# Optimization experiments

Measured on AMD Instinct MI355X. Metric: run time of the kernel, lower is better.

## Reference

```python
import jax, jax.numpy as jnp
import numpy as np

B, S, R, D_NODE, D_PAIR, N_HEAD, C = 1, 128, 256, 256, 128, 8, 32
EPS = 1e-5


def layer_norm(x, g, b):
    mu = jnp.mean(x, axis=-1, keepdims=True)
    var = jnp.mean(jnp.square(x - mu), axis=-1, keepdims=True)
    return (x - mu) * jax.lax.rsqrt(var + EPS) * g + b


def self_attention(x, qkv_w, qkv_b, gate_w, gate_b, o_w, o_b, bias=None):
    # x: [B, n1, n2, d]; attends over n2. heads: n_head x c, n_head*c == d.
    b_, n1, n2, d = x.shape
    qkv = x @ qkv_w.T + qkv_b                      # [B, n1, n2, 3*h*c]
    q, k, v = jnp.split(qkv, 3, axis=-1)
    split_heads = lambda t: t.reshape(b_, n1, n2, N_HEAD, C).transpose(0, 1, 3, 2, 4)  # [B,n1,h,n2,c]
    q = split_heads(q) * (C ** -0.5)
    k = split_heads(k)
    v = split_heads(v)
    logits = jnp.einsum('bshqc,bshkc->bshqk', q, k)  # [B, n1, h, n2, n2]
    if bias is not None:
        logits = logits + bias[:, None]              # bias: [B, h, n2, n2]
    w = jax.nn.softmax(logits, axis=-1)
    o = jnp.einsum('bshqk,bshkc->bshqc', w, v)
    o = o.transpose(0, 1, 3, 2, 4).reshape(b_, n1, n2, N_HEAD * C)
    gate = jax.nn.sigmoid(x @ gate_w.T + gate_b)
    o = o * gate
    out = o @ o_w.T
    if o_b is not None:
        out = out + o_b
    return out


def setup_inputs() -> dict:
    key = jax.random.key(0)
    ks = jax.random.split(key, 12)
    rn = lambda k, sh, sc=1.0: jax.random.normal(k, sh, dtype=jnp.float32) * sc
    return {
        'node': rn(ks[0], (B, S, R, D_NODE)),
        'pair': rn(ks[1], (B, R, R, D_PAIR)),
        'ln_mr_g': jnp.ones((D_NODE,), jnp.float32), 'ln_mr_b': jnp.zeros((D_NODE,), jnp.float32),
        'ln_z_g': jnp.ones((D_PAIR,), jnp.float32), 'ln_z_b': jnp.zeros((D_PAIR,), jnp.float32),
        'b_weights': rn(ks[2], (N_HEAD, D_PAIR), D_PAIR ** -0.5),
        'row_qkv_w': rn(ks[3], (3 * N_HEAD * C, D_NODE), D_NODE ** -0.5),
        'row_qkv_b': jnp.zeros((3 * N_HEAD * C,), jnp.float32),
        'row_gate_w': rn(ks[4], (N_HEAD * C, D_NODE), D_NODE ** -0.5),
        'row_gate_b': jnp.ones((N_HEAD * C,), jnp.float32),
        'row_o_w': rn(ks[5], (D_NODE, N_HEAD * C), D_NODE ** -0.5),
        'out_bias': jnp.zeros((D_NODE,), jnp.float32),
        'ln_mc_g': jnp.ones((D_NODE,), jnp.float32), 'ln_mc_b': jnp.zeros((D_NODE,), jnp.float32),
        'col_qkv_w': rn(ks[6], (3 * N_HEAD * C, D_NODE), D_NODE ** -0.5),
        'col_qkv_b': jnp.zeros((3 * N_HEAD * C,), jnp.float32),
        'col_gate_w': rn(ks[7], (N_HEAD * C, D_NODE), D_NODE ** -0.5),
        'col_gate_b': jnp.ones((N_HEAD * C,), jnp.float32),
        'col_o_w': rn(ks[8], (D_NODE, N_HEAD * C), D_NODE ** -0.5),
        'col_o_b': jnp.zeros((D_NODE,), jnp.float32),
        'ln_t_g': jnp.ones((D_NODE,), jnp.float32), 'ln_t_b': jnp.zeros((D_NODE,), jnp.float32),
        't_w1': rn(ks[9], (4 * D_NODE, D_NODE), D_NODE ** -0.5),
        't_b1': jnp.zeros((4 * D_NODE,), jnp.float32),
        't_w2': rn(ks[10], (D_NODE, 4 * D_NODE), (4 * D_NODE) ** -0.5),
        't_b2': jnp.zeros((D_NODE,), jnp.float32),
    }


def reference(node, pair, ln_mr_g, ln_mr_b, ln_z_g, ln_z_b, b_weights,
              row_qkv_w, row_qkv_b, row_gate_w, row_gate_b, row_o_w, out_bias,
              ln_mc_g, ln_mc_b, col_qkv_w, col_qkv_b, col_gate_w, col_gate_b, col_o_w, col_o_b,
              ln_t_g, ln_t_b, t_w1, t_b1, t_w2, t_b2):
    # --- MSARowAttentionWithPairBias ---
    M = layer_norm(node, ln_mr_g, ln_mr_b)                 # [B,S,R,D]
    Z = layer_norm(pair, ln_z_g, ln_z_b)                   # [B,R,R,Dp]
    b = jnp.einsum('bqkd,hd->bhqk', Z, b_weights)          # pair bias [B,h,R,R]
    M = self_attention(M, row_qkv_w, row_qkv_b, row_gate_w, row_gate_b, row_o_w, None, bias=b)
    # bias_dropout_add with ones dropout mask (inference): residual + (x + bias)
    node = node + M + out_bias
    # --- MSAColumnAttention ---
    Mt = node.transpose(0, 2, 1, 3)                        # [B,R,S,D], attend over S
    Mt = layer_norm(Mt, ln_mc_g, ln_mc_b)
    Mt = self_attention(Mt, col_qkv_w, col_qkv_b, col_gate_w, col_gate_b, col_o_w, col_o_b)
    node = node + Mt.transpose(0, 2, 1, 3)
    # --- MSATransition (n=4) ---
    x = layer_norm(node, ln_t_g, ln_t_b)
    x = jax.nn.relu(x @ t_w1.T + t_b1) @ t_w2.T + t_b2
    return node + x
```

## Files before the change

### kernel.cpp

```cpp
#include <hip/hip_runtime.h>
#include <hip/hip_bf16.h>

#define EPS 1e-5f

typedef __hip_bfloat16 bf16;
typedef __attribute__((ext_vector_type(8))) short short8v;
typedef __attribute__((ext_vector_type(4))) short short4v;
typedef __attribute__((ext_vector_type(4))) float f32x4;

__device__ inline f32x4 mfma16bf(short4v a, short4v b, f32x4 c) {
#if __has_builtin(__builtin_amdgcn_mfma_f32_16x16x16bf16_1k)
  return __builtin_amdgcn_mfma_f32_16x16x16bf16_1k(a, b, c, 0, 0, 0);
#else
  short8v a8 = {a[0], a[1], a[2], a[3], 0, 0, 0, 0};
  short8v b8 = {b[0], b[1], b[2], b[3], 0, 0, 0, 0};
  return __builtin_amdgcn_mfma_f32_16x16x32_bf16(a8, b8, c, 0, 0, 0);
#endif
}

__device__ inline void load_lds16(const void* g, void* l) {
  __builtin_amdgcn_global_load_lds(
      (const __attribute__((address_space(1))) void*)g,
      (__attribute__((address_space(3))) void*)l, 16, 0, 0);
}

__device__ inline unsigned pack_bf16x2(float a, float b) {
  union { bf16 h[2]; unsigned u; } cv;
  cv.h[0] = __float2bfloat16(a);
  cv.h[1] = __float2bfloat16(b);
  return cv.u;
}

struct CvtArgs {
  const float* src[8];
  bf16* dst[8];
  int n4[8];
};

__global__ __launch_bounds__(256) void cvt_all_kernel(CvtArgs a) {
  int i = blockIdx.x * 256 + threadIdx.x;
#pragma unroll
  for (int s = 0; s < 8; ++s) {
    if (i < a.n4[s]) {
      float4 v = reinterpret_cast<const float4*>(a.src[s])[i];
      union { ushort4 u; bf16 h[4]; } cv;
      cv.h[0] = __float2bfloat16(v.x);
      cv.h[1] = __float2bfloat16(v.y);
      cv.h[2] = __float2bfloat16(v.z);
      cv.h[3] = __float2bfloat16(v.w);
      reinterpret_cast<ushort4*>(a.dst[s])[i] = cv.u;
      return;
    }
    i -= a.n4[s];
  }
}

__global__ __launch_bounds__(256) void bias_concat_kernel(
    const float* rq, const float* rg, const float* cq, const float* cg,
    float* br, float* bc) {
  int i = blockIdx.x * 256 + threadIdx.x;
  if (i < 1024) {
    br[i] = (i < 768) ? rq[i] : rg[i - 768];
  } else {
    int j = i - 1024;
    bc[j] = (j < 768) ? cq[j] : cg[j - 768];
  }
}

__global__ __launch_bounds__(512) void ln256_bf_kernel(
    const float* __restrict__ in, bf16* __restrict__ out,
    const float* __restrict__ g, const float* __restrict__ b) {
  int tid = threadIdx.x;
  int w = tid >> 6, lane = tid & 63;
  int row0 = blockIdx.x * 16 + w * 2;
  const float4* r0 = reinterpret_cast<const float4*>(in + (size_t)row0 * 256);
  const float4* r1 =
      reinterpret_cast<const float4*>(in + (size_t)(row0 + 1) * 256);
  float4 x0 = r0[lane];
  float4 x1 = r1[lane];
  float4 gv = reinterpret_cast<const float4*>(g)[lane];
  float4 bv = reinterpret_cast<const float4*>(b)[lane];

  float s0 = x0.x + x0.y + x0.z + x0.w;
  float q0 = x0.x * x0.x + x0.y * x0.y + x0.z * x0.z + x0.w * x0.w;
  float s1 = x1.x + x1.y + x1.z + x1.w;
  float q1 = x1.x * x1.x + x1.y * x1.y + x1.z * x1.z + x1.w * x1.w;
#pragma unroll
  for (int off = 32; off >= 1; off >>= 1) {
    s0 += __shfl_xor(s0, off);
    q0 += __shfl_xor(q0, off);
    s1 += __shfl_xor(s1, off);
    q1 += __shfl_xor(q1, off);
  }
  float m0 = s0 * (1.0f / 256.0f);
  float i0 = rsqrtf(q0 * (1.0f / 256.0f) - m0 * m0 + EPS);
  float m1 = s1 * (1.0f / 256.0f);
  float i1 = rsqrtf(q1 * (1.0f / 256.0f) - m1 * m1 + EPS);

  union { ushort4 u; bf16 h[4]; } c0, c1;
  c0.h[0] = __float2bfloat16((x0.x - m0) * i0 * gv.x + bv.x);
  c0.h[1] = __float2bfloat16((x0.y - m0) * i0 * gv.y + bv.y);
  c0.h[2] = __float2bfloat16((x0.z - m0) * i0 * gv.z + bv.z);
  c0.h[3] = __float2bfloat16((x0.w - m0) * i0 * gv.w + bv.w);
  c1.h[0] = __float2bfloat16((x1.x - m1) * i1 * gv.x + bv.x);
  c1.h[1] = __float2bfloat16((x1.y - m1) * i1 * gv.y + bv.y);
  c1.h[2] = __float2bfloat16((x1.z - m1) * i1 * gv.z + bv.z);
  c1.h[3] = __float2bfloat16((x1.w - m1) * i1 * gv.w + bv.w);
  reinterpret_cast<ushort4*>(out + (size_t)row0 * 256)[lane] = c0.u;
  reinterpret_cast<ushort4*>(out + (size_t)(row0 + 1) * 256)[lane] = c1.u;
}

__global__ __launch_bounds__(256) void pair_bias_kernel(
    const float* __restrict__ pair, const float* __restrict__ g,
    const float* __restrict__ b, const float* __restrict__ bw,
    bf16* __restrict__ bT) {
  int tid = threadIdx.x;
  int w = tid >> 6, lane = tid & 63;
  int l15 = lane & 15, l4 = lane >> 4;
  int rowbase = blockIdx.x * 64 + w * 16;
  const float* zrow = pair + (size_t)(rowbase + l15) * 128;

  float z[4][8];
#pragma unroll
  for (int kk = 0; kk < 4; ++kk) {
    float4 a0 = *reinterpret_cast<const float4*>(zrow + kk * 32 + l4 * 8);
    float4 a1 = *reinterpret_cast<const float4*>(zrow + kk * 32 + l4 * 8 + 4);
    z[kk][0] = a0.x; z[kk][1] = a0.y; z[kk][2] = a0.z; z[kk][3] = a0.w;
    z[kk][4] = a1.x; z[kk][5] = a1.y; z[kk][6] = a1.z; z[kk][7] = a1.w;
  }
  float s = 0.0f, sq = 0.0f;
#pragma unroll
  for (int kk = 0; kk < 4; ++kk)
#pragma unroll
    for (int e = 0; e < 8; ++e) {
      s += z[kk][e];
      sq += z[kk][e] * z[kk][e];
    }
  s += __shfl_xor(s, 16);
  s += __shfl_xor(s, 32);
  sq += __shfl_xor(sq, 16);
  sq += __shfl_xor(sq, 32);
  float mu = s * (1.0f / 128.0f);
  float inv = rsqrtf(sq * (1.0f / 128.0f) - mu * mu + EPS);

  f32x4 acc = {0.f, 0.f, 0.f, 0.f};
#pragma unroll
  for (int kk = 0; kk < 4; ++kk) {
    const float* gp = g + kk * 32 + l4 * 8;
    const float* bp = b + kk * 32 + l4 * 8;
    float4 g0 = *reinterpret_cast<const float4*>(gp);
    float4 g1 = *reinterpret_cast<const float4*>(gp + 4);
    float4 b0 = *reinterpret_cast<const float4*>(bp);
    float4 b1 = *reinterpret_cast<const float4*>(bp + 4);
    float gv[8] = {g0.x, g0.y, g0.z, g0.w, g1.x, g1.y, g1.z, g1.w};
    float bv[8] = {b0.x, b0.y, b0.z, b0.w, b1.x, b1.y, b1.z, b1.w};
    union { short8v v; bf16 h[8]; } af;
#pragma unroll
    for (int e = 0; e < 8; ++e)
      af.h[e] = __float2bfloat16((z[kk][e] - mu) * inv * gv[e] + bv[e]);
    union { short8v v; bf16 h[8]; } bwf;
    if (l15 < 8) {
      const float* wp = bw + l15 * 128 + kk * 32 + l4 * 8;
      float4 w0 = *reinterpret_cast<const float4*>(wp);
      float4 w1 = *reinterpret_cast<const float4*>(wp + 4);
      float wv[8] = {w0.x, w0.y, w0.z, w0.w, w1.x, w1.y, w1.z, w1.w};
#pragma unroll
      for (int e = 0; e < 8; ++e) bwf.h[e] = __float2bfloat16(wv[e]);
    } else {
      bwf.v = short8v{0, 0, 0, 0, 0, 0, 0, 0};
    }
    acc = __builtin_amdgcn_mfma_f32_16x16x32_bf16(af.v, bwf.v, acc, 0, 0, 0);
  }
  if (l15 < 8) {
#pragma unroll
    for (int r = 0; r < 4; ++r)
      bT[(size_t)l15 * 65536 + rowbase + l4 * 4 + r] =
          __float2bfloat16(acc[r]);
  }
}

template <int EPI, int AMAP, int OMAP>
__global__ __launch_bounds__(256) void gemm_mfma_kernel(
    const bf16* __restrict__ A, const bf16* __restrict__ W,
    const float* __restrict__ bias, const float* __restrict__ aux, void* out,
    int N, int K, int nbn) {
  __shared__ __align__(16) short As[2][128 * 32];
  __shared__ __align__(16) short Bs[2][128 * 32];
  int nwg = gridDim.x;
  int qch = nwg >> 3;
  int flat = blockIdx.x;
  int wg = (flat & 7) * qch + (flat >> 3);
  int bm = wg / nbn, bn = wg % nbn;
  int tid = threadIdx.x;
  int w = tid >> 6, lane = tid & 63;
  int wr = w >> 1, wc = w & 1;
  int c0 = w * 64 + lane;
  int srow = c0 >> 2, skq = c0 & 3;
  const short* Aptr = (const short*)A;
  const short* Wbase = (const short*)(W + (size_t)(bn * 128) * K);
  f32x4 acc[4][4] = {};
  int lrow = lane & 15, kq = lane >> 4;

  auto arow = [&](int r) -> size_t {
    return AMAP ? ((size_t)r * 256 + bm) : ((size_t)(bm * 128 + r));
  };
  auto stage = [&](int buf, int k0) {
    load_lds16(Aptr + arow(srow) * K + k0 + skq * 8, &As[buf][c0 * 8]);
    load_lds16(Aptr + arow(srow + 64) * K + k0 + skq * 8,
               &As[buf][(256 + c0) * 8]);
    load_lds16(Wbase + (size_t)srow * K + k0 + skq * 8, &Bs[buf][c0 * 8]);
    load_lds16(Wbase + (size_t)(srow + 64) * K + k0 + skq * 8,
               &Bs[buf][(256 + c0) * 8]);
  };

  stage(0, 0);
  __syncthreads();
  int nk = K >> 5;
  for (int t = 0; t < nk; ++t) {
    int cur = t & 1;
    if (t + 1 < nk) stage(cur ^ 1, (t + 1) << 5);
    short8v af[4], bfv[4];
#pragma unroll
    for (int i = 0; i < 4; ++i)
      af[i] = *reinterpret_cast<const short8v*>(
          &As[cur][(wr * 64 + i * 16 + lrow) * 32 + kq * 8]);
#pragma unroll
    for (int j = 0; j < 4; ++j)
      bfv[j] = *reinterpret_cast<const short8v*>(
          &Bs[cur][(wc * 64 + j * 16 + lrow) * 32 + kq * 8]);
#pragma unroll
    for (int i = 0; i < 4; ++i)
#pragma unroll
      for (int j = 0; j < 4; ++j)
        acc[i][j] = __builtin_amdgcn_mfma_f32_16x16x32_bf16(af[i], bfv[j],
                                                            acc[i][j], 0, 0, 0);
    __syncthreads();
  }

  float* outF = (float*)out;
  bf16* outB = (bf16*)out;
  int r4 = (lane >> 4) * 4;
#pragma unroll
  for (int j = 0; j < 4; ++j) {
    int c = bn * 128 + wc * 64 + j * 16 + lrow;
    float bv = bias ? bias[c] : 0.0f;
#pragma unroll
    for (int i = 0; i < 4; ++i) {
      int lr0 = wr * 64 + i * 16 + r4;
#pragma unroll
      for (int reg = 0; reg < 4; ++reg) {
        int lr = lr0 + reg;
        size_t off = OMAP ? (((size_t)lr * 256 + bm) * N + c)
                          : ((size_t)(bm * 128 + lr) * N + c);
        float v = acc[i][j][reg] + bv;
        if (EPI == 0) {
          outB[off] = __float2bfloat16(v);
        } else if (EPI == 2) {
          outF[off] = v + aux[off];
        } else {
          outB[off] = __float2bfloat16(fmaxf(v, 0.0f));
        }
      }
    }
  }
}

template <bool ROWMODE>
__global__ __launch_bounds__(512) void attn_mfma_kernel(
    const bf16* __restrict__ qkv, const bf16* __restrict__ bT,
    bf16* __restrict__ o) {
  constexpr int KVLEN = ROWMODE ? 256 : 128;
  constexpr int QT = ROWMODE ? 2 : 1;
  constexpr int KOUT = KVLEN / 64;
  constexpr int STRIDE = 1024;
  constexpr int NT = 512;
  __shared__ __align__(16) short K_lds[KVLEN * 32];
  __shared__ __align__(16) short Vt_lds[32 * KVLEN];

  int b = blockIdx.x;
  int idx = b >> 3, h = b & 7;
  const short* qb = (const short*)qkv + (size_t)idx * (KVLEN * 1024);
  const bf16* qbh = (const bf16*)qb;
  bf16* ob = o + (size_t)idx * (KVLEN * 256);
  int tid = threadIdx.x;
  int w = tid >> 6, lane = tid & 63;
  int l15 = lane & 15, l4 = lane >> 4;

#pragma unroll
  for (int rnd = 0; rnd < (KVLEN * 4) / NT; ++rnd) {
    int c = rnd * NT + tid;
    int row = c >> 2;
    int kq = (c & 3) ^ ((row >> 1) & 3);
    load_lds16(qb + (size_t)row * STRIDE + 256 + h * 32 + kq * 8,
               &K_lds[c * 8]);
  }
  {
    int tt = tid;
    if (KVLEN * 2 == NT || tt < KVLEN * 2) {
      int kp = tt >> 2;
      int cc = (tt & 3) * 8;
      short8v va = *reinterpret_cast<const short8v*>(
          qb + (size_t)(2 * kp) * STRIDE + 512 + h * 32 + cc);
      short8v vb = *reinterpret_cast<const short8v*>(
          qb + (size_t)(2 * kp + 1) * STRIDE + 512 + h * 32 + cc);
      int k = 2 * kp;
      int u = k >> 3;
      int klo = k & 7;
#pragma unroll
      for (int e = 0; e < 8; ++e) {
        int cI = cc + e;
        int up = u ^ (cI & 7);
        unsigned pk = (unsigned)(unsigned short)va[e] |
                      ((unsigned)(unsigned short)vb[e] << 16);
        *reinterpret_cast<unsigned*>(&Vt_lds[cI * KVLEN + up * 8 + klo]) = pk;
      }
    }
  }
  __syncthreads();

  int q0 = w * QT * 16;
  short8v qf[QT];
#pragma unroll
  for (int j = 0; j < QT; ++j)
    qf[j] = *reinterpret_cast<const short8v*>(
        qb + (size_t)(q0 + j * 16 + l15) * STRIDE + h * 32 + l4 * 8);

  float lrun[QT];
#pragma unroll
  for (int j = 0; j < QT; ++j) lrun[j] = 0.0f;
  f32x4 acc_o[QT][2] = {};

  const float SC = 0.17677669529663687f;
  const float L2E = 1.4426950408889634f;
  const f32x4 zf = {0.f, 0.f, 0.f, 0.f};

#pragma unroll 1
  for (int kt = 0; kt < KOUT; ++kt) {
    ushort4 bb[QT][4];
    if (ROWMODE) {
#pragma unroll
      for (int j = 0; j < QT; ++j) {
        const bf16* bq = bT + (size_t)h * 65536 +
                         (size_t)(q0 + j * 16 + l15) * 256 + kt * 64 + l4 * 4;
#pragma unroll
        for (int i = 0; i < 4; ++i)
          bb[j][i] = *reinterpret_cast<const ushort4*>(bq + i * 16);
      }
    }
    short8v kf[4];
#pragma unroll
    for (int i = 0; i < 4; ++i) {
      int krow = kt * 64 + i * 16 + l15;
      kf[i] = *reinterpret_cast<const short8v*>(
          &K_lds[krow * 32 + ((l4 ^ ((krow >> 1) & 3)) * 8)]);
    }
    short4v vfa[4][2];
#pragma unroll
    for (int ks4 = 0; ks4 < 4; ++ks4)
#pragma unroll
      for (int ct = 0; ct < 2; ++ct) {
        int cI = ct * 16 + l15;
        int u = kt * 8 + ks4 * 2 + (l4 >> 1);
        vfa[ks4][ct] = *reinterpret_cast<const short4v*>(
            &Vt_lds[cI * KVLEN + (u ^ (cI & 7)) * 8 + (l4 & 1) * 4]);
      }

#pragma unroll
    for (int j = 0; j < QT; ++j) {
      f32x4 accs[4];
#pragma unroll
      for (int i = 0; i < 4; ++i)
        accs[i] =
            __builtin_amdgcn_mfma_f32_16x16x32_bf16(kf[i], qf[j], zf, 0, 0, 0);
      float sum = 0.0f;
#pragma unroll
      for (int i = 0; i < 4; ++i) {
        if (ROWMODE) {
          union { ushort4 u; bf16 h4[4]; } bu;
          bu.u = bb[j][i];
#pragma unroll
          for (int r = 0; r < 4; ++r)
            accs[i][r] = accs[i][r] * SC + __bfloat162float(bu.h4[r]);
        } else {
#pragma unroll
          for (int r = 0; r < 4; ++r) accs[i][r] *= SC;
        }
#pragma unroll
        for (int r = 0; r < 4; ++r) {
          float p = exp2f(accs[i][r] * L2E);
          accs[i][r] = p;
          sum += p;
        }
      }
      sum += __shfl_xor(sum, 16);
      sum += __shfl_xor(sum, 32);
      lrun[j] += sum;
#pragma unroll
      for (int ks4 = 0; ks4 < 4; ++ks4) {
        union { unsigned u2[2]; short4v s; } pb;
        pb.u2[0] = pack_bf16x2(accs[ks4][0], accs[ks4][1]);
        pb.u2[1] = pack_bf16x2(accs[ks4][2], accs[ks4][3]);
#pragma unroll
        for (int ct = 0; ct < 2; ++ct)
          acc_o[j][ct] = mfma16bf(vfa[ks4][ct], pb.s, acc_o[j][ct]);
      }
    }
  }

#pragma unroll
  for (int j = 0; j < QT; ++j) {
    float inv = 1.0f / lrun[j];
    int row = q0 + j * 16 + l15;
    const bf16* grow = qbh + (size_t)row * STRIDE + 768 + h * 32;
    bf16* orow = ob + (size_t)row * 256 + h * 32;
#pragma unroll
    for (int ct = 0; ct < 2; ++ct) {
      int cc = ct * 16 + l4 * 4;
      ushort4 gv = *reinterpret_cast<const ushort4*>(grow + cc);
      union { ushort4 u; bf16 h4[4]; } gu, ou;
      gu.u = gv;
#pragma unroll
      for (int r = 0; r < 4; ++r) {
        float gt = __bfloat162float(gu.h4[r]);
        float sg = 1.0f / (1.0f + __expf(-gt));
        ou.h4[r] = __float2bfloat16(acc_o[j][ct][r] * inv * sg);
      }
      *reinterpret_cast<ushort4*>(orow + cc) = ou.u;
    }
  }
}

extern "C" void kernel_launch(void* const* d_in, const int* in_sizes, int n_in,
                              void* d_out, int out_size, void* d_ws,
                              size_t ws_size, hipStream_t stream) {
  (void)in_sizes; (void)n_in; (void)out_size; (void)ws_size;
  const float* node      = (const float*)d_in[0];
  const float* pair      = (const float*)d_in[1];
  const float* ln_mr_g   = (const float*)d_in[2];
  const float* ln_mr_b   = (const float*)d_in[3];
  const float* ln_z_g    = (const float*)d_in[4];
  const float* ln_z_b    = (const float*)d_in[5];
  const float* b_weights = (const float*)d_in[6];
  const float* row_qkv_w = (const float*)d_in[7];
  const float* row_qkv_b = (const float*)d_in[8];
  const float* row_gate_w= (const float*)d_in[9];
  const float* row_gate_b= (const float*)d_in[10];
  const float* row_o_w   = (const float*)d_in[11];
  const float* out_bias  = (const float*)d_in[12];
  const float* ln_mc_g   = (const float*)d_in[13];
  const float* ln_mc_b   = (const float*)d_in[14];
  const float* col_qkv_w = (const float*)d_in[15];
  const float* col_qkv_b = (const float*)d_in[16];
  const float* col_gate_w= (const float*)d_in[17];
  const float* col_gate_b= (const float*)d_in[18];
  const float* col_o_w   = (const float*)d_in[19];
  const float* col_o_b   = (const float*)d_in[20];
  const float* ln_t_g    = (const float*)d_in[21];
  const float* ln_t_b    = (const float*)d_in[22];
  const float* t_w1      = (const float*)d_in[23];
  const float* t_b1      = (const float*)d_in[24];
  const float* t_w2      = (const float*)d_in[25];
  const float* t_b2      = (const float*)d_in[26];
  float* out = (float*)d_out;

  const size_t NR = 32768;
  char* p = (char*)d_ws;
  float* buf_node = (float*)p; p += NR * 256 * 4;
  char*  qkv_region = p;       p += NR * 1024 * 2;
  bf16* buf_bias  = (bf16*)p;  p += 8 * 256 * 256 * 2;
  bf16* ln_bf     = (bf16*)p;  p += NR * 256 * 2;
  bf16* g_bf      = (bf16*)p;  p += NR * 256 * 2;
  bf16* qkv_bf = (bf16*)qkv_region;
  bf16* h_bf   = (bf16*)qkv_region;
  bf16* w_rqkvg = (bf16*)p; p += 1024 * 256 * 2;
  bf16* w_ro    = (bf16*)p; p += 256 * 256 * 2;
  bf16* w_cqkvg = (bf16*)p; p += 1024 * 256 * 2;
  bf16* w_co    = (bf16*)p; p += 256 * 256 * 2;
  bf16* w_t1    = (bf16*)p; p += 1024 * 256 * 2;
  bf16* w_t2    = (bf16*)p; p += 256 * 1024 * 2;
  float* b_rqkvg = (float*)p; p += 1024 * 4;
  float* b_cqkvg = (float*)p; p += 1024 * 4;

  CvtArgs ca;
  ca.src[0] = row_qkv_w;  ca.dst[0] = w_rqkvg;             ca.n4[0] = 49152;
  ca.src[1] = row_gate_w; ca.dst[1] = w_rqkvg + 768 * 256; ca.n4[1] = 16384;
  ca.src[2] = row_o_w;    ca.dst[2] = w_ro;                ca.n4[2] = 16384;
  ca.src[3] = col_qkv_w;  ca.dst[3] = w_cqkvg;             ca.n4[3] = 49152;
  ca.src[4] = col_gate_w; ca.dst[4] = w_cqkvg + 768 * 256; ca.n4[4] = 16384;
  ca.src[5] = col_o_w;    ca.dst[5] = w_co;                ca.n4[5] = 16384;
  ca.src[6] = t_w1;       ca.dst[6] = w_t1;                ca.n4[6] = 65536;
  ca.src[7] = t_w2;       ca.dst[7] = w_t2;                ca.n4[7] = 65536;
  cvt_all_kernel<<<1152, 256, 0, stream>>>(ca);
  bias_concat_kernel<<<8, 256, 0, stream>>>(row_qkv_b, row_gate_b, col_qkv_b,
                                            col_gate_b, b_rqkvg, b_cqkvg);

  ln256_bf_kernel<<<2048, 512, 0, stream>>>(node, ln_bf, ln_mr_g, ln_mr_b);
  pair_bias_kernel<<<1024, 256, 0, stream>>>(pair, ln_z_g, ln_z_b, b_weights,
                                             buf_bias);
  gemm_mfma_kernel<0, 0, 0><<<2048, 256, 0, stream>>>(
      ln_bf, w_rqkvg, b_rqkvg, nullptr, qkv_bf, 1024, 256, 8);
  attn_mfma_kernel<true><<<1024, 512, 0, stream>>>(qkv_bf, buf_bias, g_bf);
  gemm_mfma_kernel<2, 0, 0><<<512, 256, 0, stream>>>(
      g_bf, w_ro, out_bias, node, buf_node, 256, 256, 2);

  ln256_bf_kernel<<<2048, 512, 0, stream>>>(buf_node, ln_bf, ln_mc_g, ln_mc_b);
  gemm_mfma_kernel<0, 1, 0><<<2048, 256, 0, stream>>>(
      ln_bf, w_cqkvg, b_cqkvg, nullptr, qkv_bf, 1024, 256, 8);
  attn_mfma_kernel<false><<<2048, 512, 0, stream>>>(qkv_bf, nullptr, g_bf);
  gemm_mfma_kernel<2, 0, 1><<<512, 256, 0, stream>>>(
      g_bf, w_co, col_o_b, buf_node, buf_node, 256, 256, 2);

  ln256_bf_kernel<<<2048, 512, 0, stream>>>(buf_node, ln_bf, ln_t_g, ln_t_b);
  gemm_mfma_kernel<3, 0, 0><<<2048, 256, 0, stream>>>(
      ln_bf, w_t1, t_b1, nullptr, h_bf, 1024, 256, 8);
  gemm_mfma_kernel<2, 0, 0><<<512, 256, 0, stream>>>(
      h_bf, w_t2, t_b2, buf_node, out, 256, 1024, 2);
}
```

Before: 305.5 us.

## Fold query scale into weights, inject pair bias via MFMA accumulator, sum rows with MFMA

The 1/sqrt(C) query scale is folded into the Q rows of the QKV weights and biases during conversion, which removes the per-logit multiply. The pair bias is now stored as fp32 and loaded straight into the MFMA accumulator input, so no separate add and bf16 unpack is needed. The softmax row sum is computed by an extra MFMA against a ones vector instead of scalar adds plus cross-lane shuffles. In exchange, bias reads double in bytes and each key step issues an extra MFMA.

```diff
diff --git a/kernel.cpp b/kernel.cpp
--- a/kernel.cpp
+++ b/kernel.cpp
@@ -31,10 +31,13 @@
   return cv.u;
 }
 
+#define QSCALE 0.17677669529663687f
+
 struct CvtArgs {
   const float* src[8];
   bf16* dst[8];
   int n4[8];
+  int scale_n4[8];
 };
 
 __global__ __launch_bounds__(256) void cvt_all_kernel(CvtArgs a) {
@@ -43,11 +46,12 @@
   for (int s = 0; s < 8; ++s) {
     if (i < a.n4[s]) {
       float4 v = reinterpret_cast<const float4*>(a.src[s])[i];
+      float sc = (i < a.scale_n4[s]) ? QSCALE : 1.0f;
       union { ushort4 u; bf16 h[4]; } cv;
-      cv.h[0] = __float2bfloat16(v.x);
-      cv.h[1] = __float2bfloat16(v.y);
-      cv.h[2] = __float2bfloat16(v.z);
-      cv.h[3] = __float2bfloat16(v.w);
+      cv.h[0] = __float2bfloat16(v.x * sc);
+      cv.h[1] = __float2bfloat16(v.y * sc);
+      cv.h[2] = __float2bfloat16(v.z * sc);
+      cv.h[3] = __float2bfloat16(v.w * sc);
       reinterpret_cast<ushort4*>(a.dst[s])[i] = cv.u;
       return;
     }
@@ -60,10 +64,12 @@
     float* br, float* bc) {
   int i = blockIdx.x * 256 + threadIdx.x;
   if (i < 1024) {
-    br[i] = (i < 768) ? rq[i] : rg[i - 768];
+    float v = (i < 768) ? rq[i] : rg[i - 768];
+    br[i] = (i < 256) ? v * QSCALE : v;
   } else {
     int j = i - 1024;
-    bc[j] = (j < 768) ? cq[j] : cg[j - 768];
+    float v = (j < 768) ? cq[j] : cg[j - 768];
+    bc[j] = (j < 256) ? v * QSCALE : v;
   }
 }
 
@@ -113,7 +119,7 @@
 __global__ __launch_bounds__(256) void pair_bias_kernel(
     const float* __restrict__ pair, const float* __restrict__ g,
     const float* __restrict__ b, const float* __restrict__ bw,
-    bf16* __restrict__ bT) {
+    float* __restrict__ bT) {
   int tid = threadIdx.x;
   int w = tid >> 6, lane = tid & 63;
   int l15 = lane & 15, l4 = lane >> 4;
@@ -174,8 +180,7 @@
   if (l15 < 8) {
 #pragma unroll
     for (int r = 0; r < 4; ++r)
-      bT[(size_t)l15 * 65536 + rowbase + l4 * 4 + r] =
-          __float2bfloat16(acc[r]);
+      bT[(size_t)l15 * 65536 + rowbase + l4 * 4 + r] = acc[r];
   }
 }
 
@@ -267,7 +272,7 @@
 
 template <bool ROWMODE>
 __global__ __launch_bounds__(512) void attn_mfma_kernel(
-    const bf16* __restrict__ qkv, const bf16* __restrict__ bT,
+    const bf16* __restrict__ qkv, const float* __restrict__ bT,
     bf16* __restrict__ o) {
   constexpr int KVLEN = ROWMODE ? 256 : 128;
   constexpr int QT = ROWMODE ? 2 : 1;
@@ -325,26 +330,24 @@
     qf[j] = *reinterpret_cast<const short8v*>(
         qb + (size_t)(q0 + j * 16 + l15) * STRIDE + h * 32 + l4 * 8);
 
-  float lrun[QT];
-#pragma unroll
-  for (int j = 0; j < QT; ++j) lrun[j] = 0.0f;
   f32x4 acc_o[QT][2] = {};
-
-  const float SC = 0.17677669529663687f;
+  f32x4 acc_l[QT] = {};
+  const short4v ones = {0x3F80, 0x3F80, 0x3F80, 0x3F80};
+
   const float L2E = 1.4426950408889634f;
   const f32x4 zf = {0.f, 0.f, 0.f, 0.f};
 
 #pragma unroll 1
   for (int kt = 0; kt < KOUT; ++kt) {
-    ushort4 bb[QT][4];
+    float4 bb[QT][4];
     if (ROWMODE) {
 #pragma unroll
       for (int j = 0; j < QT; ++j) {
-        const bf16* bq = bT + (size_t)h * 65536 +
-                         (size_t)(q0 + j * 16 + l15) * 256 + kt * 64 + l4 * 4;
+        const float* bq = bT + (size_t)h * 65536 +
+                          (size_t)(q0 + j * 16 + l15) * 256 + kt * 64 + l4 * 4;
 #pragma unroll
         for (int i = 0; i < 4; ++i)
-          bb[j][i] = *reinterpret_cast<const ushort4*>(bq + i * 16);
+          bb[j][i] = *reinterpret_cast<const float4*>(bq + i * 16);
       }
     }
     short8v kf[4];
@@ -369,32 +372,22 @@
     for (int j = 0; j < QT; ++j) {
       f32x4 accs[4];
 #pragma unroll
+      for (int i = 0; i < 4; ++i) {
+        f32x4 cin = zf;
+        if (ROWMODE) {
+          cin[0] = bb[j][i].x;
+          cin[1] = bb[j][i].y;
+          cin[2] = bb[j][i].z;
+          cin[3] = bb[j][i].w;
+        }
+        accs[i] =
+            __builtin_amdgcn_mfma_f32_16x16x32_bf16(kf[i], qf[j], cin, 0, 0, 0);
+      }
+#pragma unroll
       for (int i = 0; i < 4; ++i)
-        accs[i] =
-            __builtin_amdgcn_mfma_f32_16x16x32_bf16(kf[i], qf[j], zf, 0, 0, 0);
-      float sum = 0.0f;
-#pragma unroll
-      for (int i = 0; i < 4; ++i) {
-        if (ROWMODE) {
-          union { ushort4 u; bf16 h4[4]; } bu;
-          bu.u = bb[j][i];
-#pragma unroll
-          for (int r = 0; r < 4; ++r)
-            accs[i][r] = accs[i][r] * SC + __bfloat162float(bu.h4[r]);
-        } else {
-#pragma unroll
-          for (int r = 0; r < 4; ++r) accs[i][r] *= SC;
-        }
-#pragma unroll
-        for (int r = 0; r < 4; ++r) {
-          float p = exp2f(accs[i][r] * L2E);
-          accs[i][r] = p;
-          sum += p;
-        }
-      }
-      sum += __shfl_xor(sum, 16);
-      sum += __shfl_xor(sum, 32);
-      lrun[j] += sum;
+#pragma unroll
+        for (int r = 0; r < 4; ++r)
+          accs[i][r] = exp2f(accs[i][r] * L2E);
 #pragma unroll
       for (int ks4 = 0; ks4 < 4; ++ks4) {
         union { unsigned u2[2]; short4v s; } pb;
@@ -403,13 +396,14 @@
 #pragma unroll
         for (int ct = 0; ct < 2; ++ct)
           acc_o[j][ct] = mfma16bf(vfa[ks4][ct], pb.s, acc_o[j][ct]);
+        acc_l[j] = mfma16bf(ones, pb.s, acc_l[j]);
       }
     }
   }
 
 #pragma unroll
   for (int j = 0; j < QT; ++j) {
-    float inv = 1.0f / lrun[j];
+    float inv = 1.0f / acc_l[j][0];
     int row = q0 + j * 16 + l15;
     const bf16* grow = qbh + (size_t)row * STRIDE + 768 + h * 32;
     bf16* orow = ob + (size_t)row * 256 + h * 32;
@@ -467,7 +461,7 @@
   char* p = (char*)d_ws;
   float* buf_node = (float*)p; p += NR * 256 * 4;
   char*  qkv_region = p;       p += NR * 1024 * 2;
-  bf16* buf_bias  = (bf16*)p;  p += 8 * 256 * 256 * 2;
+  float* buf_bias = (float*)p; p += 8 * 256 * 256 * 4;
   bf16* ln_bf     = (bf16*)p;  p += NR * 256 * 2;
   bf16* g_bf      = (bf16*)p;  p += NR * 256 * 2;
   bf16* qkv_bf = (bf16*)qkv_region;
@@ -490,6 +484,9 @@
   ca.src[5] = col_o_w;    ca.dst[5] = w_co;                ca.n4[5] = 16384;
   ca.src[6] = t_w1;       ca.dst[6] = w_t1;                ca.n4[6] = 65536;
   ca.src[7] = t_w2;       ca.dst[7] = w_t2;                ca.n4[7] = 65536;
+  for (int s = 0; s < 8; ++s) ca.scale_n4[s] = 0;
+  ca.scale_n4[0] = 16384;
+  ca.scale_n4[3] = 16384;
   cvt_all_kernel<<<1152, 256, 0, stream>>>(ca);
   bias_concat_kernel<<<8, 256, 0, stream>>>(row_qkv_b, row_gate_b, col_qkv_b,
                                             col_gate_b, b_rqkvg, b_cqkvg);
```

Result: no change. 303.2 us (-0.8%).
